# Performance work log

Hardware: AMD Instinct MI355X
Metric: run time of the kernel (lower is better)

## Reference

```python
import jax, jax.numpy as jnp
import numpy as np

B, NX, NT, W, M = 4, 512, 128, 64, 16
EPS = 1e-5


def setup_inputs() -> dict:
    key = jax.random.key(0)
    ks = jax.random.split(key, 13)
    scale = 1.0 / (W * W)  # torch: scale * torch.rand(..., cfloat) -> U[0,1) real & imag
    return {
        "x": jax.random.normal(ks[0], (B, NX, NT, W), jnp.float32),
        "grid": jnp.linspace(0.0, 1.0, NX, dtype=jnp.float32),
        "pole_re": scale * jax.random.uniform(ks[1], (W, W, M), jnp.float32),
        "pole_im": scale * jax.random.uniform(ks[2], (W, W, M), jnp.float32),
        "res_re": scale * jax.random.uniform(ks[3], (W, W, M), jnp.float32),
        "res_im": scale * jax.random.uniform(ks[4], (W, W, M), jnp.float32),
        "conv_w": jax.random.normal(ks[5], (W, W), jnp.float32) / np.sqrt(W),
        "conv_b": jax.random.normal(ks[6], (W,), jnp.float32) * 0.02,
        "gru_Wx": jax.random.normal(ks[7], (3 * W, W), jnp.float32) / np.sqrt(W),
        "gru_Wh": jax.random.normal(ks[8], (3 * W, W), jnp.float32) / np.sqrt(W),
        "gru_bx": jax.random.normal(ks[9], (3 * W,), jnp.float32) * 0.02,
        "gru_bh": jax.random.normal(ks[10], (3 * W,), jnp.float32) * 0.02,
        "out_W": jax.random.normal(ks[11], (W, W), jnp.float32) / np.sqrt(W),
        "out_b": jax.random.normal(ks[12], (W,), jnp.float32) * 0.02,
    }


def instance_norm(v):
    # torch InstanceNorm1d (affine=False, biased var) over last dim; v: [N, C, L]
    mu = v.mean(-1, keepdims=True)
    var = ((v - mu) ** 2).mean(-1, keepdims=True)
    return (v - mu) * jax.lax.rsqrt(var + EPS)


def pr_forward(xs, grid, pole, residue):
    # xs: [BT, W, Nx]; pole/residue: [in, out, modes] complex64
    nx = xs.shape[-1]
    dt = grid[1] - grid[0]
    alpha = jnp.fft.fft(xs)  # [BT, W, Nx] complex64
    lam = 1j * (2.0 * np.pi) * jnp.fft.fftfreq(nx, dt).astype(jnp.float32)  # [Nx]
    Hw = residue / (lam[:, None, None, None] - pole)  # [Nx, i, o, m]
    or1 = jnp.einsum('bix,xiom->box', alpha, Hw)       # [BT, W, Nx]
    or2 = -jnp.einsum('bix,xiom->bom', alpha, Hw)      # [BT, W, M]
    x1 = jnp.real(jnp.fft.ifft(or1, n=nx))
    # exp of outer product pole (x) grid: [i, o, m, Nx]
    term2 = jnp.exp(pole[..., None] * grid.astype(jnp.complex64)[None, None, None, :])
    # faithful to torch einsum 'bix,ioxz->boz': or2 channel contracts with term2's in-dim
    x2 = jnp.real(jnp.einsum('bim,iomz->boz', or2, term2)) / nx
    return x1 + x2


def gru(xseq, Wx, Wh, bx, bh):
    # xseq: [N, T, D] -> [N, T, H]; torch nn.GRU gate order (r, z, n)
    H = Wh.shape[1]
    gx = xseq @ Wx.T + bx  # precompute input gates [N, T, 3H]

    def step(h, g):
        gh = h @ Wh.T + bh
        xr, xz, xn = jnp.split(g, 3, axis=-1)
        hr, hz, hn = jnp.split(gh, 3, axis=-1)
        r = jax.nn.sigmoid(xr + hr)
        z = jax.nn.sigmoid(xz + hz)
        n = jnp.tanh(xn + r * hn)
        h = (1.0 - z) * n + z * h
        return h, h

    h0 = jnp.zeros((xseq.shape[0], H), xseq.dtype)
    _, hs = jax.lax.scan(step, h0, gx.transpose(1, 0, 2))
    return hs.transpose(1, 0, 2)


def reference(x, grid, pole_re, pole_im, res_re, res_im, conv_w, conv_b,
              gru_Wx, gru_Wh, gru_bx, gru_bh, out_W, out_b):
    b, nx, nt, w = x.shape
    xs = x.transpose(0, 2, 3, 1).reshape(b * nt, w, nx)  # [B*Nt, W, Nx]
    pole = pole_re + 1j * pole_im
    residue = res_re + 1j * res_im
    x1 = instance_norm(pr_forward(instance_norm(xs), grid, pole, residue))
    x2 = jnp.einsum('oi,bin->bon', conv_w, xs) + conv_b[None, :, None]  # Conv1d k=1
    h = jnp.sin(x1 + x2)
    h = h.reshape(b, nt, w, nx).transpose(0, 3, 1, 2).reshape(b * nx, nt, w)
    y = gru(h, gru_Wx, gru_Wh, gru_bx, gru_bh) @ out_W.T + out_b
    return y.reshape(b, nx, nt, w)
```

## Files before the change

kernel.cpp:

```cpp
#include <hip/hip_runtime.h>
#include <math.h>

#define PI2F 6.283185307179586f


__global__ __launch_bounds__(256) void k1a_transpose(const float* __restrict__ x,
                                                     float* __restrict__ xs) {
  const int bt = blockIdx.x >> 2, nt4 = blockIdx.x & 3;
  const int b = bt >> 7, t = bt & 127;
  const int n0 = nt4 * 128;
  __shared__ float tile[128 * 66];
  const int tid = threadIdx.x;
  const int i = tid & 63, nq = tid >> 6;
  const float* xb = x + (size_t)b * 4194304 + (size_t)t * 64;
  for (int k = 0; k < 32; k++) {
    int nl = nq + 4 * k;
    tile[nl * 66 + i] = xb[(size_t)(n0 + nl) * 8192 + i];
  }
  __syncthreads();
  float* dst = xs + (size_t)bt * 32768;
  for (int idx = tid; idx < 8192; idx += 256) {
    int ii = idx >> 7, nl = idx & 127;
    dst[ii * 512 + n0 + nl] = tile[nl * 66 + ii];
  }
}

__global__ __launch_bounds__(64) void k2_fft(const float* __restrict__ xs,
                                             float2* __restrict__ alpha,
                                             float2* __restrict__ a0,
                                             float2* __restrict__ a256,
                                             float2* __restrict__ s1o,
                                             float2* __restrict__ s2o,
                                             const float* __restrict__ grd) {
  __shared__ float2 bufA[512], bufB[512], tw[256];
  const int s = blockIdx.x, tid = threadIdx.x;
  const float dt = grd[1] - grd[0];
  const float Ndt = 512.f * dt;
  for (int m = tid; m < 256; m += 64) {
    float ang = -PI2F * (float)m * (1.f / 512.f);
    float sv, cv; sincosf(ang, &sv, &cv);
    tw[m].x = cv; tw[m].y = sv;
  }
  const float* src = xs + (size_t)s * 512;
  float v[8]; float sm = 0.f, sq = 0.f;
#pragma unroll
  for (int k = 0; k < 8; k++) { v[k] = src[tid + 64 * k]; sm += v[k]; sq += v[k] * v[k]; }
#pragma unroll
  for (int off = 32; off; off >>= 1) { sm += __shfl_down(sm, off); sq += __shfl_down(sq, off); }
  sm = __shfl(sm, 0); sq = __shfl(sq, 0);
  float mu = sm * (1.f / 512.f);
  float var = sq * (1.f / 512.f) - mu * mu;
  float rs = rsqrtf(var + 1e-5f);
#pragma unroll
  for (int k = 0; k < 8; k++) { bufA[tid + 64 * k].x = (v[k] - mu) * rs; bufA[tid + 64 * k].y = 0.f; }
  __syncthreads();
  float2* sp = bufA; float2* dp = bufB;
  int Ns = 1;
  for (int st = 0; st < 9; st++) {
    const int shift = 8 - st;
    for (int jj = 0; jj < 4; jj++) {
      int j = tid + 64 * jj;
      int r = j & (Ns - 1);
      float2 a = sp[j], b = sp[j + 256];
      float2 w = tw[r << shift];
      float wbx = w.x * b.x - w.y * b.y;
      float wby = w.x * b.y + w.y * b.x;
      int id = ((j >> st) << (st + 1)) + r;
      dp[id].x = a.x + wbx; dp[id].y = a.y + wby;
      dp[id + Ns].x = a.x - wbx; dp[id + Ns].y = a.y - wby;
    }
    __syncthreads();
    float2* tp = sp; sp = dp; dp = tp;
    Ns <<= 1;
  }
  float2* dst = alpha + (size_t)s * 256;
  float s1x = 0.f, s1y = 0.f, s2x = 0.f, s2y = 0.f;
  for (int k = tid; k < 512; k += 64) {
    float2 vv = sp[k];
    if (k < 256) dst[k] = vv;
    if (k != 0) {
      int kk = (k < 256) ? k : k - 512;
      float invL = Ndt / (PI2F * (float)kk);
      s1x += vv.y * invL; s1y -= vv.x * invL;
      float invL2 = invL * invL;
      s2x -= vv.x * invL2; s2y -= vv.y * invL2;
    }
  }
#pragma unroll
  for (int off = 32; off; off >>= 1) {
    s1x += __shfl_down(s1x, off); s1y += __shfl_down(s1y, off);
    s2x += __shfl_down(s2x, off); s2y += __shfl_down(s2y, off);
  }
  if (tid == 0) {
    s1o[s].x = s1x; s1o[s].y = s1y;
    s2o[s].x = s2x; s2o[s].y = s2y;
    a0[s] = sp[0];
    a256[s] = sp[256];
  }
}

__global__ __launch_bounds__(64) void k3a_R(const float* __restrict__ pre, const float* __restrict__ pim,
                                            const float* __restrict__ rre, const float* __restrict__ rim,
                                            float2* __restrict__ R0, float2* __restrict__ R1,
                                            float2* __restrict__ R2,
                                            float* __restrict__ Pm, float* __restrict__ Qm,
                                            float* __restrict__ ptr_re, float* __restrict__ ptr_im) {
  const int i = blockIdx.x, o = threadIdx.x;
  float r0x = 0, r0y = 0, r1x = 0, r1y = 0, r2x = 0, r2y = 0;
  for (int m = 0; m < 16; m++) {
    size_t idx = ((size_t)i * 64 + o) * 16 + m;
    float px = pre[idx], py = pim[idx];
    float rx = rre[idx], ry = rim[idx];
    r1x += rx; r1y += ry;
    r2x += rx * px - ry * py; r2y += rx * py + ry * px;
    float inv = 1.f / (px * px + py * py);
    r0x -= (rx * px + ry * py) * inv;
    r0y -= (ry * px - rx * py) * inv;
    ptr_re[((size_t)i * 16 + m) * 64 + o] = px;
    ptr_im[((size_t)i * 16 + m) * 64 + o] = py;
  }
  R0[i * 64 + o].x = r0x; R0[i * 64 + o].y = r0y;
  R1[i * 64 + o].x = r1x; R1[i * 64 + o].y = r1y;
  R2[i * 64 + o].x = r2x; R2[i * 64 + o].y = r2y;
  Pm[i * 64 + o] = 2.f * r1x;
  Qm[i * 64 + o] = 2.f * r2x;
}

__global__ __launch_bounds__(1024) void k3b_or2(const float* __restrict__ pre, const float* __restrict__ pim,
                                                const float* __restrict__ rre, const float* __restrict__ rim,
                                                const float2* __restrict__ a0, const float2* __restrict__ s1,
                                                const float2* __restrict__ s2, float2* __restrict__ or2) {
  const int bt = blockIdx.x;
  __shared__ float2 A0[64], S1[64], S2[64];
  const int tid = threadIdx.x;
  if (tid < 64) { A0[tid] = a0[bt * 64 + tid]; S1[tid] = s1[bt * 64 + tid]; S2[tid] = s2[bt * 64 + tid]; }
  __syncthreads();
  float ax = 0.f, ay = 0.f;
  for (int i = 0; i < 64; i++) {
    size_t idx = (size_t)i * 1024 + tid;
    float px = pre[idx], py = pim[idx];
    float rx = rre[idx], ry = rim[idx];
    float inv = 1.f / (px * px + py * py);
    float q0x = -(rx * px + ry * py) * inv;
    float q0y = -(ry * px - rx * py) * inv;
    float2 a0v = A0[i], s1v = S1[i], s2v = S2[i];
    float tx = q0x * a0v.x - q0y * a0v.y + rx * s1v.x - ry * s1v.y;
    float ty = q0x * a0v.y + q0y * a0v.x + rx * s1v.y + ry * s1v.x;
    float rpx = rx * px - ry * py, rpy = rx * py + ry * px;
    tx += rpx * s2v.x - rpy * s2v.y;
    ty += rpx * s2v.y + rpy * s2v.x;
    ax -= tx; ay -= ty;
  }
  or2[(size_t)bt * 1024 + tid].x = ax;
  or2[(size_t)bt * 1024 + tid].y = ay;
}

__global__ __launch_bounds__(256) void k3c_T(const float2* __restrict__ or2,
                                             const float* __restrict__ ptr_re, const float* __restrict__ ptr_im,
                                             const float2* __restrict__ R0, const float2* __restrict__ R1,
                                             const float2* __restrict__ R2,
                                             const float2* __restrict__ a0, const float2* __restrict__ a256,
                                             float* __restrict__ T0, float* __restrict__ T1,
                                             float* __restrict__ T2,
                                             float* __restrict__ or10re, float* __restrict__ r256o,
                                             const float* __restrict__ grd) {
  const int bt = blockIdx.x * 4 + (threadIdx.x >> 6);
  const int o = threadIdx.x & 63;
  const float dt = grd[1] - grd[0];
  const float invL256 = -(512.f * dt) / (PI2F * 256.f);
  float ox = 0.f;
  float c1x = 0.f, c1y = 0.f, c2x = 0.f, c2y = 0.f;
  for (int i = 0; i < 64; i++) {
    float2 av = a0[bt * 64 + i];
    float2 rv = R0[i * 64 + o];
    ox += av.x * rv.x - av.y * rv.y;
    float2 aw = a256[bt * 64 + i];
    float2 r1v = R1[i * 64 + o], r2v = R2[i * 64 + o];
    c1x += aw.x * r1v.x - aw.y * r1v.y;
    c1y += aw.x * r1v.y + aw.y * r1v.x;
    c2x += aw.x * r2v.x - aw.y * r2v.y;
    c2y += aw.x * r2v.y + aw.y * r2v.x;
  }
  or10re[bt * 64 + o] = ox;
  r256o[bt * 64 + o] = invL256 * (c1y - invL256 * c2x);
  float t0 = 0.f, t1 = 0.f, t2 = 0.f;
  for (int im = 0; im < 1024; im++) {
    float2 c = or2[(size_t)bt * 1024 + im];
    float px = ptr_re[(size_t)im * 64 + o], py = ptr_im[(size_t)im * 64 + o];
    t0 += c.x;
    t1 += c.x * px - c.y * py;
    float p2x = px * px - py * py, p2y = 2.f * px * py;
    t2 += c.x * p2x - c.y * p2y;
  }
  T1[bt * 64 + o] = t1; T2[bt * 64 + o] = t2;
  if (o == 0) T0[bt] = t0;
}

__global__ __launch_bounds__(256) void k4_or1(float2* __restrict__ alpha,
                                              const float* __restrict__ Pm, const float* __restrict__ Qm,
                                              const float* __restrict__ or10re, const float* __restrict__ r256o,
                                              const float* __restrict__ grd) {
  const int bt = blockIdx.x >> 2, xc = blockIdx.x & 3;
  const int x0 = xc * 64;
  __shared__ float aRe[64][68], aIm[64][68];
  const int tid = threadIdx.x;
  const float dt = grd[1] - grd[0];
  const float Ndt = 512.f * dt;
  float2* base = alpha + (size_t)bt * 16384;
  for (int idx = tid; idx < 4096; idx += 256) {
    int ii = idx >> 6, xl = idx & 63;
    float2 v = base[ii * 256 + x0 + xl];
    aRe[ii][xl] = v.x; aIm[ii][xl] = v.y;
  }
  __syncthreads();
  const int xq = tid & 15, oq = tid >> 4;
  const int xb = xq * 4, ob = oq * 4;
  float c1r[4][4] = {}, c1i[4][4] = {}, c2r[4][4] = {}, c2i[4][4] = {};
#pragma unroll 4
  for (int i = 0; i < 64; i++) {
    float4 ar = *(const float4*)&aRe[i][xb];
    float4 ai = *(const float4*)&aIm[i][xb];
    float4 pv = *(const float4*)&Pm[i * 64 + ob];
    float4 qv = *(const float4*)&Qm[i * 64 + ob];
    float pa[4] = {pv.x, pv.y, pv.z, pv.w};
    float qa[4] = {qv.x, qv.y, qv.z, qv.w};
    float arr[4] = {ar.x, ar.y, ar.z, ar.w};
    float aii[4] = {ai.x, ai.y, ai.z, ai.w};
#pragma unroll
    for (int a = 0; a < 4; a++) {
#pragma unroll
      for (int c = 0; c < 4; c++) {
        c1r[a][c] += arr[c] * pa[a];
        c1i[a][c] += aii[c] * pa[a];
        c2r[a][c] += arr[c] * qa[a];
        c2i[a][c] += aii[c] * qa[a];
      }
    }
  }
#pragma unroll
  for (int a = 0; a < 4; a++) {
    int o = ob + a;
    float2* orow = base + o * 256 + x0;
#pragma unroll
    for (int c = 0; c < 4; c++) {
      int gx = x0 + xb + c;
      float re, im;
      if (gx == 0) {
        re = or10re[bt * 64 + o];
        im = r256o[bt * 64 + o];
      } else {
        float invL = Ndt / (PI2F * (float)gx);
        re = invL * (c1i[a][c] - invL * c2r[a][c]);
        im = -invL * (c1r[a][c] + invL * c2i[a][c]);
      }
      orow[xb + c].x = re; orow[xb + c].y = im;
    }
  }
}

__global__ __launch_bounds__(64) void k5_ifft(const float2* __restrict__ G,
                                              float* __restrict__ x1,
                                              const float* __restrict__ T0, const float* __restrict__ T1,
                                              const float* __restrict__ T2, const float* __restrict__ grd) {
  __shared__ float2 bufA[512], bufB[512], tw[256];
  const int s = blockIdx.x, tid = threadIdx.x;
  const int bt = s >> 6;
  for (int m = tid; m < 256; m += 64) {
    float ang = PI2F * (float)m * (1.f / 512.f);
    float sv, cv; sincosf(ang, &sv, &cv);
    tw[m].x = cv; tw[m].y = sv;
  }
  const float2* src = G + (size_t)s * 256;
  float2 g0 = src[0];
  for (int k = tid; k < 512; k += 64) {
    float2 vv; vv.x = 0.f; vv.y = 0.f;
    if (k >= 1 && k < 256) vv = src[k];
    bufA[k] = vv;
  }
  __syncthreads();
  float2* sp = bufA; float2* dp = bufB;
  int Ns = 1;
  for (int st = 0; st < 9; st++) {
    const int shift = 8 - st;
    for (int jj = 0; jj < 4; jj++) {
      int j = tid + 64 * jj;
      int r = j & (Ns - 1);
      float2 a = sp[j], b = sp[j + 256];
      float2 w = tw[r << shift];
      float wbx = w.x * b.x - w.y * b.y;
      float wby = w.x * b.y + w.y * b.x;
      int id = ((j >> st) << (st + 1)) + r;
      dp[id].x = a.x + wbx; dp[id].y = a.y + wby;
      dp[id + Ns].x = a.x - wbx; dp[id + Ns].y = a.y - wby;
    }
    __syncthreads();
    float2* tp = sp; sp = dp; dp = tp;
    Ns <<= 1;
  }
  const float t0 = T0[bt], t1 = T1[s], t2 = T2[s];
  float* dst = x1 + (size_t)s * 512;
  for (int k = tid; k < 512; k += 64) {
    float g = grd[k];
    float sgn = (k & 1) ? -1.f : 1.f;
    dst[k] = (sp[k].x + g0.x + sgn * g0.y + t0 + t1 * g + 0.5f * t2 * g * g) * (1.f / 512.f);
  }
}

__global__ __launch_bounds__(256) void k6a_stats(const float* __restrict__ x1,
                                                 float* __restrict__ mu2, float* __restrict__ rs2) {
  const int row = blockIdx.x * 4 + (threadIdx.x >> 6);
  const int lane = threadIdx.x & 63;
  const float* p = x1 + (size_t)row * 512;
  float s = 0.f, s2 = 0.f;
#pragma unroll
  for (int k = 0; k < 8; k++) { float v = p[lane + 64 * k]; s += v; s2 += v * v; }
#pragma unroll
  for (int off = 32; off; off >>= 1) { s += __shfl_down(s, off); s2 += __shfl_down(s2, off); }
  if (lane == 0) {
    float mu = s * (1.f / 512.f);
    float var = s2 * (1.f / 512.f) - mu * mu;
    mu2[row] = mu;
    rs2[row] = rsqrtf(var + 1e-5f);
  }
}

__global__ __launch_bounds__(256) void k6b_assemble(const float* __restrict__ xsraw,
                                                    const float* __restrict__ x1,
                                                    const float* __restrict__ conv_w,
                                                    const float* __restrict__ conv_b,
                                                    const float* __restrict__ mu2, const float* __restrict__ rs2,
                                                    float* __restrict__ hseq) {
  const int bt = blockIdx.x >> 2, nt4 = blockIdx.x & 3;
  const int b = bt >> 7, t = bt & 127;
  const int n0 = nt4 * 128;
  __shared__ float xt[128 * 66];
  __shared__ float wt[64 * 66];
  __shared__ float mun[64], rsn[64];
  const int tid = threadIdx.x;
  for (int idx = tid; idx < 4096; idx += 256) {
    int o = idx >> 6, ii = idx & 63;
    wt[o * 66 + ii] = conv_w[idx];
  }
  if (tid < 64) { mun[tid] = mu2[bt * 64 + tid]; rsn[tid] = rs2[bt * 64 + tid]; }
  const float* src = xsraw + (size_t)bt * 32768;
  for (int idx = tid; idx < 8192; idx += 256) {
    int ii = idx >> 7, nl = idx & 127;
    xt[nl * 66 + ii] = src[ii * 512 + n0 + nl];
  }
  __syncthreads();
  const int lane = tid & 63, og = tid >> 6;
  float acc[2][16];
  for (int half = 0; half < 2; half++) {
    int nl = lane + 64 * half;
#pragma unroll
    for (int j = 0; j < 16; j++) acc[half][j] = conv_b[og * 16 + j];
    const float2* xrow = (const float2*)&xt[nl * 66];
#pragma unroll 4
    for (int i2 = 0; i2 < 32; i2++) {
      float2 v = xrow[i2];
#pragma unroll
      for (int j = 0; j < 16; j++) {
        float2 wv = *(const float2*)&wt[(og * 16 + j) * 66 + 2 * i2];
        acc[half][j] += wv.x * v.x + wv.y * v.y;
      }
    }
  }
  const float* xb = x1 + (size_t)bt * 32768 + n0;
  for (int half = 0; half < 2; half++) {
    int nl = lane + 64 * half;
#pragma unroll
    for (int j = 0; j < 16; j++) {
      int o = og * 16 + j;
      float v = (xb[o * 512 + nl] - mun[o]) * rsn[o] + acc[half][j];
      acc[half][j] = sinf(v);
    }
  }
  __syncthreads();
  float* tile = xt;
  for (int half = 0; half < 2; half++) {
    int nl = lane + 64 * half;
#pragma unroll
    for (int j = 0; j < 16; j++) tile[(og * 16 + j) * 129 + nl] = acc[half][j];
  }
  __syncthreads();
  for (int idx = tid; idx < 8192; idx += 256) {
    int nl = idx >> 6, o = idx & 63;
    hseq[(((size_t)(b * 512 + n0 + nl)) * 128 + t) * 64 + o] = tile[o * 129 + nl];
  }
}

__global__ __launch_bounds__(256) void k7_gru(const float* __restrict__ hseq,
                                              const float* __restrict__ Wx, const float* __restrict__ Wh,
                                              const float* __restrict__ bx, const float* __restrict__ bh,
                                              float* __restrict__ hist) {
  __shared__ float wstage[12288];
  __shared__ float xl[4][68], hl[4][68];
  __shared__ float axl[4][192], ahl[4][192];
  const int tid = threadIdx.x;
  const int rowb = blockIdx.x * 4;
  float wx[64], wh[64];
  for (int idx = tid; idx < 12288; idx += 256) wstage[idx] = Wx[idx];
  __syncthreads();
  if (tid < 192) {
#pragma unroll
    for (int c = 0; c < 64; c++) wx[c] = wstage[tid * 64 + c];
  }
  __syncthreads();
  for (int idx = tid; idx < 12288; idx += 256) wstage[idx] = Wh[idx];
  __syncthreads();
  if (tid < 192) {
#pragma unroll
    for (int c = 0; c < 64; c++) wh[c] = wstage[tid * 64 + c];
  }
  const float bxg = (tid < 192) ? bx[tid] : 0.f;
  const float bhg = (tid < 192) ? bh[tid] : 0.f;
  if (tid < 64) { hl[0][tid] = 0.f; hl[1][tid] = 0.f; hl[2][tid] = 0.f; hl[3][tid] = 0.f; }
  __syncthreads();
  const int r_ = tid >> 6, c_ = tid & 63;
  for (int t = 0; t < 128; t++) {
    xl[r_][c_] = hseq[((size_t)(rowb + r_) * 128 + t) * 64 + c_];
    __syncthreads();
    if (tid < 192) {
#pragma unroll
      for (int r = 0; r < 4; r++) {
        float ax = bxg, ah = bhg;
#pragma unroll
        for (int c4 = 0; c4 < 16; c4++) {
          float4 xv = *(const float4*)&xl[r][c4 * 4];
          float4 hv = *(const float4*)&hl[r][c4 * 4];
          ax += wx[4 * c4] * xv.x + wx[4 * c4 + 1] * xv.y + wx[4 * c4 + 2] * xv.z + wx[4 * c4 + 3] * xv.w;
          ah += wh[4 * c4] * hv.x + wh[4 * c4 + 1] * hv.y + wh[4 * c4 + 2] * hv.z + wh[4 * c4 + 3] * hv.w;
        }
        axl[r][tid] = ax; ahl[r][tid] = ah;
      }
    }
    __syncthreads();
    if (tid < 64) {
#pragma unroll
      for (int r = 0; r < 4; r++) {
        float xr = axl[r][c_],       hr = ahl[r][c_];
        float xz = axl[r][64 + c_],  hz = ahl[r][64 + c_];
        float xn = axl[r][128 + c_], hn = ahl[r][128 + c_];
        float rg = 1.f / (1.f + expf(-(xr + hr)));
        float zg = 1.f / (1.f + expf(-(xz + hz)));
        float ng = tanhf(xn + rg * hn);
        float hv = (1.f - zg) * ng + zg * hl[r][c_];
        hl[r][c_] = hv;
        hist[((size_t)(rowb + r) * 128 + t) * 64 + c_] = hv;
      }
    }
    __syncthreads();
  }
}

__global__ __launch_bounds__(256) void k8_out(const float* __restrict__ hist,
                                              const float* __restrict__ outW, const float* __restrict__ outb,
                                              float* __restrict__ y) {
  __shared__ float ht[64 * 68];
  __shared__ float wl[4096];
  const int tid = threadIdx.x;
  const int rt0 = blockIdx.x * 64;
  for (int idx = tid; idx < 4096; idx += 256) wl[idx] = outW[idx];
  for (int idx = tid; idx < 4096; idx += 256) {
    int rt = idx >> 6, c = idx & 63;
    ht[rt * 68 + c] = hist[(size_t)(rt0 + rt) * 64 + c];
  }
  __syncthreads();
  const int j = tid & 63, rg = tid >> 6;
  float wj[64];
#pragma unroll
  for (int c = 0; c < 64; c++) wj[c] = wl[j * 64 + c];
  const float bj = outb[j];
  for (int k = 0; k < 16; k++) {
    int rt = rg + 4 * k;
    float acc = bj;
    const float4* hp = (const float4*)&ht[rt * 68];
#pragma unroll
    for (int c4 = 0; c4 < 16; c4++) {
      float4 hv = hp[c4];
      acc += wj[4 * c4] * hv.x + wj[4 * c4 + 1] * hv.y + wj[4 * c4 + 2] * hv.z + wj[4 * c4 + 3] * hv.w;
    }
    y[(size_t)(rt0 + rt) * 64 + j] = acc;
  }
}

extern "C" void kernel_launch(void* const* d_in, const int* in_sizes, int n_in,
                              void* d_out, int out_size, void* d_ws, size_t ws_size,
                              hipStream_t stream) {
  (void)in_sizes; (void)n_in; (void)out_size;
  const float* x      = (const float*)d_in[0];
  const float* grd    = (const float*)d_in[1];
  const float* pre    = (const float*)d_in[2];
  const float* pim    = (const float*)d_in[3];
  const float* rre    = (const float*)d_in[4];
  const float* rim    = (const float*)d_in[5];
  const float* conv_w = (const float*)d_in[6];
  const float* conv_b = (const float*)d_in[7];
  const float* gWx    = (const float*)d_in[8];
  const float* gWh    = (const float*)d_in[9];
  const float* gbx    = (const float*)d_in[10];
  const float* gbh    = (const float*)d_in[11];
  const float* outW   = (const float*)d_in[12];
  const float* outb   = (const float*)d_in[13];
  float* out = (float*)d_out;
  float* ws  = (float*)d_ws;

  if (ws_size < 52003328ULL * 4ULL) return;

  float*  XS = ws;
  float2* AH = (float2*)(ws + 16777216);
  float*  X1 = ws + 33554432;
  float*  sm = ws + 50331648;
  float2* A0    = (float2*)(sm + 0);
  float2* A256  = (float2*)(sm + 65536);
  float2* S1    = (float2*)(sm + 131072);
  float2* S2    = (float2*)(sm + 196608);
  float2* R0    = (float2*)(sm + 262144);
  float2* R1C   = (float2*)(sm + 270336);
  float2* R2C   = (float2*)(sm + 278528);
  float*  Pm    = sm + 286720;
  float*  Qm    = sm + 290816;
  float*  PTR   = sm + 294912;
  float*  PTI   = sm + 360448;
  float2* OR2   = (float2*)(sm + 425984);
  float*  T0    = sm + 1474560;
  float*  T1    = sm + 1475072;
  float*  T2    = sm + 1507840;
  float*  OR10R = sm + 1540608;
  float*  R256  = sm + 1573376;
  float*  MU2   = sm + 1606144;
  float*  RS2   = sm + 1638912;

  float* hseq = (float*)AH;
  float* hist = X1;

  k1a_transpose<<<2048, 256, 0, stream>>>(x, XS);
  k2_fft<<<32768, 64, 0, stream>>>(XS, AH, A0, A256, S1, S2, grd);
  k3a_R<<<64, 64, 0, stream>>>(pre, pim, rre, rim, R0, R1C, R2C, Pm, Qm, PTR, PTI);
  k3b_or2<<<512, 1024, 0, stream>>>(pre, pim, rre, rim, A0, S1, S2, OR2);
  k3c_T<<<128, 256, 0, stream>>>(OR2, PTR, PTI, R0, R1C, R2C, A0, A256, T0, T1, T2, OR10R, R256, grd);
  k4_or1<<<2048, 256, 0, stream>>>(AH, Pm, Qm, OR10R, R256, grd);
  k5_ifft<<<32768, 64, 0, stream>>>(AH, X1, T0, T1, T2, grd);
  k6a_stats<<<8192, 256, 0, stream>>>(X1, MU2, RS2);
  k6b_assemble<<<2048, 256, 0, stream>>>(XS, X1, conv_w, conv_b, MU2, RS2, hseq);
  k7_gru<<<512, 256, 0, stream>>>(hseq, gWx, gWh, gbx, gbh, hist);
  k8_out<<<4096, 256, 0, stream>>>(hist, outW, outb, out);
}
```

Before: 1.266 ms.

## Rewrite GRU kernel as one wavefront per sequence using lane shuffles

The GRU recurrence is rebuilt so each 64-thread block (one wavefront) handles a single sequence. Each thread keeps all six gate weight rows for its output unit in registers and broadcasts h and x across lanes with __shfl, which removes LDS staging and the three __syncthreads per timestep. The next input is prefetched one step ahead, and fast __expf-based sigmoid and tanh replace expf and tanhf. In exchange, each thread holds 384 weight registers, which risks spills or very low occupancy, and the fast-math exponentials slightly change accuracy.

```diff
diff --git a/kernel.cpp b/kernel.cpp
--- a/kernel.cpp
+++ b/kernel.cpp
@@ -389,67 +389,61 @@
   }
 }
 
-__global__ __launch_bounds__(256) void k7_gru(const float* __restrict__ hseq,
-                                              const float* __restrict__ Wx, const float* __restrict__ Wh,
-                                              const float* __restrict__ bx, const float* __restrict__ bh,
-                                              float* __restrict__ hist) {
-  __shared__ float wstage[12288];
-  __shared__ float xl[4][68], hl[4][68];
-  __shared__ float axl[4][192], ahl[4][192];
-  const int tid = threadIdx.x;
-  const int rowb = blockIdx.x * 4;
-  float wx[64], wh[64];
-  for (int idx = tid; idx < 12288; idx += 256) wstage[idx] = Wx[idx];
-  __syncthreads();
-  if (tid < 192) {
-#pragma unroll
-    for (int c = 0; c < 64; c++) wx[c] = wstage[tid * 64 + c];
-  }
-  __syncthreads();
-  for (int idx = tid; idx < 12288; idx += 256) wstage[idx] = Wh[idx];
-  __syncthreads();
-  if (tid < 192) {
-#pragma unroll
-    for (int c = 0; c < 64; c++) wh[c] = wstage[tid * 64 + c];
-  }
-  const float bxg = (tid < 192) ? bx[tid] : 0.f;
-  const float bhg = (tid < 192) ? bh[tid] : 0.f;
-  if (tid < 64) { hl[0][tid] = 0.f; hl[1][tid] = 0.f; hl[2][tid] = 0.f; hl[3][tid] = 0.f; }
-  __syncthreads();
-  const int r_ = tid >> 6, c_ = tid & 63;
+__global__ __launch_bounds__(64) void k7_gru(const float* __restrict__ hseq,
+                                             const float* __restrict__ Wx, const float* __restrict__ Wh,
+                                             const float* __restrict__ bx, const float* __restrict__ bh,
+                                             float* __restrict__ hist) {
+  const int row = blockIdx.x;
+  const int j = threadIdx.x;
+  float wxr[64], wxz[64], wxn[64], whr[64], whz[64], whn[64];
+  {
+    const float4* pr = (const float4*)(Wx + (size_t)j * 64);
+    const float4* pz = (const float4*)(Wx + (size_t)(j + 64) * 64);
+    const float4* pn = (const float4*)(Wx + (size_t)(j + 128) * 64);
+    const float4* qr = (const float4*)(Wh + (size_t)j * 64);
+    const float4* qz = (const float4*)(Wh + (size_t)(j + 64) * 64);
+    const float4* qn = (const float4*)(Wh + (size_t)(j + 128) * 64);
+#pragma unroll
+    for (int c4 = 0; c4 < 16; c4++) {
+      float4 v;
+      v = pr[c4]; wxr[4*c4]=v.x; wxr[4*c4+1]=v.y; wxr[4*c4+2]=v.z; wxr[4*c4+3]=v.w;
+      v = pz[c4]; wxz[4*c4]=v.x; wxz[4*c4+1]=v.y; wxz[4*c4+2]=v.z; wxz[4*c4+3]=v.w;
+      v = pn[c4]; wxn[4*c4]=v.x; wxn[4*c4+1]=v.y; wxn[4*c4+2]=v.z; wxn[4*c4+3]=v.w;
+      v = qr[c4]; whr[4*c4]=v.x; whr[4*c4+1]=v.y; whr[4*c4+2]=v.z; whr[4*c4+3]=v.w;
+      v = qz[c4]; whz[4*c4]=v.x; whz[4*c4+1]=v.y; whz[4*c4+2]=v.z; whz[4*c4+3]=v.w;
+      v = qn[c4]; whn[4*c4]=v.x; whn[4*c4+1]=v.y; whn[4*c4+2]=v.z; whn[4*c4+3]=v.w;
+    }
+  }
+  const float br  = bx[j] + bh[j];
+  const float bz  = bx[j + 64] + bh[j + 64];
+  const float bxn = bx[j + 128];
+  const float bhn = bh[j + 128];
+  const float* xrow = hseq + (size_t)row * 8192;
+  float* hrow = hist + (size_t)row * 8192;
+  float h = 0.f;
+  float xcur = xrow[j];
   for (int t = 0; t < 128; t++) {
-    xl[r_][c_] = hseq[((size_t)(rowb + r_) * 128 + t) * 64 + c_];
-    __syncthreads();
-    if (tid < 192) {
-#pragma unroll
-      for (int r = 0; r < 4; r++) {
-        float ax = bxg, ah = bhg;
-#pragma unroll
-        for (int c4 = 0; c4 < 16; c4++) {
-          float4 xv = *(const float4*)&xl[r][c4 * 4];
-          float4 hv = *(const float4*)&hl[r][c4 * 4];
-          ax += wx[4 * c4] * xv.x + wx[4 * c4 + 1] * xv.y + wx[4 * c4 + 2] * xv.z + wx[4 * c4 + 3] * xv.w;
-          ah += wh[4 * c4] * hv.x + wh[4 * c4 + 1] * hv.y + wh[4 * c4 + 2] * hv.z + wh[4 * c4 + 3] * hv.w;
-        }
-        axl[r][tid] = ax; ahl[r][tid] = ah;
-      }
-    }
-    __syncthreads();
-    if (tid < 64) {
-#pragma unroll
-      for (int r = 0; r < 4; r++) {
-        float xr = axl[r][c_],       hr = ahl[r][c_];
-        float xz = axl[r][64 + c_],  hz = ahl[r][64 + c_];
-        float xn = axl[r][128 + c_], hn = ahl[r][128 + c_];
-        float rg = 1.f / (1.f + expf(-(xr + hr)));
-        float zg = 1.f / (1.f + expf(-(xz + hz)));
-        float ng = tanhf(xn + rg * hn);
-        float hv = (1.f - zg) * ng + zg * hl[r][c_];
-        hl[r][c_] = hv;
-        hist[((size_t)(rowb + r) * 128 + t) * 64 + c_] = hv;
-      }
-    }
-    __syncthreads();
+    float xnext = (t < 127) ? xrow[(t + 1) * 64 + j] : 0.f;
+    float aR = br, aZ = bz, aXN = bxn, aHN = bhn;
+#pragma unroll
+    for (int c = 0; c < 64; c++) {
+      float hc = __shfl(h, c);
+      float xc = __shfl(xcur, c);
+      aR  += whr[c] * hc;
+      aR  += wxr[c] * xc;
+      aZ  += whz[c] * hc;
+      aZ  += wxz[c] * xc;
+      aXN += wxn[c] * xc;
+      aHN += whn[c] * hc;
+    }
+    float r = 1.f / (1.f + __expf(-aR));
+    float z = 1.f / (1.f + __expf(-aZ));
+    float nv = aXN + r * aHN;
+    float e2 = __expf(2.f * nv);
+    float th = 1.f - 2.f / (e2 + 1.f);
+    h = (1.f - z) * th + z * h;
+    hrow[t * 64 + j] = h;
+    xcur = xnext;
   }
 }
 
@@ -543,6 +537,6 @@
   k5_ifft<<<32768, 64, 0, stream>>>(AH, X1, T0, T1, T2, grd);
   k6a_stats<<<8192, 256, 0, stream>>>(X1, MU2, RS2);
   k6b_assemble<<<2048, 256, 0, stream>>>(XS, X1, conv_w, conv_b, MU2, RS2, hseq);
-  k7_gru<<<512, 256, 0, stream>>>(hseq, gWx, gWh, gbx, gbh, hist);
+  k7_gru<<<2048, 64, 0, stream>>>(hseq, gWx, gWh, gbx, gbh, hist);
   k8_out<<<4096, 256, 0, stream>>>(hist, outW, outb, out);
 }
```

After: 1.534 ms. +21.1%, slower.
